# Performance work log

Hardware: AMD Instinct MI355X
Metric: run time of the kernel (lower is better)

The kernel has to match this reference:

```python
import jax, jax.numpy as jnp
import numpy as np

N_NODES = 50000
N_EDGES = 500000
HIDDEN = 128
HEADS = 8
HEAD_DIM = HIDDEN // HEADS


def setup_inputs() -> dict:
    key = jax.random.key(0)
    ks = jax.random.split(key, 20)

    def lin_w(k, fin, fout):
        return (jax.random.normal(k, (fin, fout), jnp.float32) / np.sqrt(fin)).astype(jnp.float32)

    inp = {
        "h": jax.random.normal(ks[0], (N_NODES, HIDDEN), jnp.float32),
        "x": jax.random.normal(ks[1], (N_NODES, 3), jnp.float32),
        "src": jax.random.randint(ks[2], (N_EDGES,), 0, N_NODES, jnp.int32),
        "dst": jax.random.randint(ks[3], (N_EDGES,), 0, N_NODES, jnp.int32),
        "distances": jax.random.uniform(ks[4], (N_EDGES,), jnp.float32),
        # linear layers stored as [in, out] (transposed vs torch nn.Linear)
        "Wq": lin_w(ks[5], HIDDEN, HIDDEN), "bq": jnp.zeros((HIDDEN,), jnp.float32),
        "Wk": lin_w(ks[6], HIDDEN, HIDDEN), "bk": jnp.zeros((HIDDEN,), jnp.float32),
        "Wv": lin_w(ks[7], HIDDEN, HIDDEN), "bv": jnp.zeros((HIDDEN,), jnp.float32),
        "Wo": lin_w(ks[8], HIDDEN, HIDDEN), "bo": jnp.zeros((HIDDEN,), jnp.float32),
        "Wd": lin_w(ks[9], 1, HEADS), "bd": jnp.zeros((HEADS,), jnp.float32),
        "Wg1": lin_w(ks[10], HIDDEN, HIDDEN), "bg1": jnp.zeros((HIDDEN,), jnp.float32),
        "Wg2": lin_w(ks[11], HIDDEN, 1), "bg2": jnp.zeros((1,), jnp.float32),
    }
    return inp


def reference(h, x, src, dst, distances,
              Wq, bq, Wk, bk, Wv, bv, Wo, bo, Wd, bd, Wg1, bg1, Wg2, bg2):
    n = h.shape[0]
    heads = Wd.shape[1]
    dh = Wq.shape[1] // heads

    q = (h @ Wq + bq).reshape(n, heads, dh)
    k = (h @ Wk + bk).reshape(n, heads, dh)
    v = (h @ Wv + bv).reshape(n, heads, dh)

    q_src = q[src]            # [E, heads, dh]
    k_dst = k[dst]
    v_dst = v[dst]

    logits = jnp.einsum('ehd,ehd->eh', q_src, k_dst) / jnp.sqrt(jnp.asarray(dh, h.dtype))
    bias = (distances * distances)[:, None] @ Wd + bd      # [E, heads]
    lg = logits - bias

    # segment softmax over edges grouped by src node
    m = jax.ops.segment_max(lg, src, num_segments=n)        # [N, heads]
    ex = jnp.exp(lg - m[src])
    s = jax.ops.segment_sum(ex, src, num_segments=n)
    w = ex / jnp.maximum(s[src], 1e-9)                      # [E, heads]

    h_upd = jax.ops.segment_sum(v_dst * w[:, :, None], src, num_segments=n)
    h_out = h + h_upd.reshape(n, heads * dh) @ Wo + bo

    w_mean = w.mean(axis=1)                                 # mean over heads -> [E]
    disp = jax.ops.segment_sum((x[dst] - x[src]) * w_mean[:, None], src, num_segments=n)

    gate = jnp.tanh(jax.nn.silu(h_out @ Wg1 + bg1) @ Wg2 + bg2)  # [N, 1]
    x_out = x + gate * disp
    return (h_out, x_out)
```

## Files before the change

kernel.cpp:

```cpp
#include <hip/hip_runtime.h>
#include <math.h>

#define N_NODES 50000
#define N_EDGES 500000
#define HIDDEN 128
#define HEADS 8
#define HEAD_DIM 16

typedef __attribute__((ext_vector_type(8))) short short8;
typedef __attribute__((ext_vector_type(4))) float floatx4;
typedef __attribute__((ext_vector_type(4))) unsigned short ushort4v;

#define OFF_Q       0u
#define OFF_KV      6400000u
#define OFF_HHI     12800000u
#define OFF_HLO     16000000u
#define OFF_DISP    19200000u
#define OFF_CNT     19350016u
#define OFF_ROWPTR  19400032u
#define OFF_CURSOR  19450048u
#define OFF_ESD     19500064u
#define OFF_WSPLIT  20500064u

static __device__ __forceinline__ unsigned short f2bf(float f) {
    unsigned u = __builtin_bit_cast(unsigned, f);
    unsigned r = (u + 0x7FFFu + ((u >> 16) & 1u)) >> 16;
    return (unsigned short)r;
}
static __device__ __forceinline__ float bf2f(unsigned short s) {
    return __builtin_bit_cast(float, (unsigned)s << 16);
}

__global__ void k_zero_int(int* __restrict__ p, int n) {
    int i = blockIdx.x * 256 + threadIdx.x;
    if (i < n) p[i] = 0;
}

__global__ __launch_bounds__(256) void k_split_h(
    const float* __restrict__ h,
    unsigned short* __restrict__ hhi, unsigned short* __restrict__ hlo) {
    int i = (blockIdx.x * 256 + threadIdx.x) * 4;
    float4 xv = *(const float4*)(h + i);
    ushort4v hi, lo;
    float v0[4] = {xv.x, xv.y, xv.z, xv.w};
#pragma unroll
    for (int j = 0; j < 4; ++j) {
        unsigned short a = f2bf(v0[j]);
        hi[j] = a;
        lo[j] = f2bf(v0[j] - bf2f(a));
    }
    *(ushort4v*)(hhi + i) = hi;
    *(ushort4v*)(hlo + i) = lo;
}

__global__ void k_split_w(const float* __restrict__ Wq, const float* __restrict__ Wk,
                          const float* __restrict__ Wv, const float* __restrict__ Wo,
                          const float* __restrict__ Wg1, unsigned short* __restrict__ ws) {
    int t = blockIdx.x * 256 + threadIdx.x;
    int m = t >> 14, r = t & 16383;
    int k = r >> 7, n = r & 127;
    const float* W = (m == 0) ? Wq : (m == 1) ? Wk : (m == 2) ? Wv : (m == 3) ? Wo : Wg1;
    float x = W[k * 128 + n];
    int kc = k >> 5, kin = k & 31, quad = kin >> 3, j = kin & 7;
    int ct = n >> 4, nin = n & 15, lane = quad * 16 + nin;
    unsigned base = ((((unsigned)(m * 4 + kc) * 8 + ct) * 2) * 64 + lane) * 8 + j;
    unsigned short a = f2bf(x);
    ws[base] = a;
    ws[base + 512] = f2bf(x - bf2f(a));
}

__global__ __launch_bounds__(256) void k_qkv_mfma(
    const unsigned short* __restrict__ hhi, const unsigned short* __restrict__ hlo,
    const unsigned short* __restrict__ wsp,
    const float* __restrict__ bq, const float* __restrict__ bk, const float* __restrict__ bv,
    float* __restrict__ q, unsigned* __restrict__ kvp) {
    const int wave = threadIdx.x >> 6, lane = threadIdx.x & 63;
    const int quad = lane >> 4, l15 = lane & 15;
    const int ct0 = wave * 2;
    const int row0 = blockIdx.x * 32;

    floatx4 acc[3][2][2];
#pragma unroll
    for (int m = 0; m < 3; ++m)
#pragma unroll
        for (int c = 0; c < 2; ++c)
#pragma unroll
            for (int r = 0; r < 2; ++r) acc[m][c][r] = (floatx4){0.f, 0.f, 0.f, 0.f};

#pragma unroll
    for (int kc = 0; kc < 4; ++kc) {
        short8 ah[2], al[2];
#pragma unroll
        for (int rt = 0; rt < 2; ++rt) {
            int row = row0 + rt * 16 + l15;
            if (row >= N_NODES) row = N_NODES - 1;
            size_t off = (size_t)row * 128 + kc * 32 + quad * 8;
            ah[rt] = *(const short8*)(hhi + off);
            al[rt] = *(const short8*)(hlo + off);
        }
#pragma unroll
        for (int m = 0; m < 3; ++m) {
#pragma unroll
            for (int ctl = 0; ctl < 2; ++ctl) {
                unsigned fb = ((((unsigned)(m * 4 + kc) * 8 + (ct0 + ctl)) * 2) * 64 + lane) * 8;
                short8 bh = *(const short8*)(wsp + fb);
                short8 bl = *(const short8*)(wsp + fb + 512);
#pragma unroll
                for (int rt = 0; rt < 2; ++rt) {
                    acc[m][ctl][rt] = __builtin_amdgcn_mfma_f32_16x16x32_bf16(
                        ah[rt], bh, acc[m][ctl][rt], 0, 0, 0);
                    acc[m][ctl][rt] = __builtin_amdgcn_mfma_f32_16x16x32_bf16(
                        ah[rt], bl, acc[m][ctl][rt], 0, 0, 0);
                    acc[m][ctl][rt] = __builtin_amdgcn_mfma_f32_16x16x32_bf16(
                        al[rt], bh, acc[m][ctl][rt], 0, 0, 0);
                }
            }
        }
    }

#pragma unroll
    for (int ctl = 0; ctl < 2; ++ctl) {
        int col = (ct0 + ctl) * 16 + l15;
        float bq_ = bq[col], bk_ = bk[col], bv_ = bv[col];
#pragma unroll
        for (int rt = 0; rt < 2; ++rt) {
#pragma unroll
            for (int reg = 0; reg < 4; ++reg) {
                int row = row0 + rt * 16 + quad * 4 + reg;
                if (row < N_NODES) {
                    q[(size_t)row * 128 + col] = acc[0][ctl][rt][reg] + bq_;
                    unsigned kb = f2bf(acc[1][ctl][rt][reg] + bk_);
                    unsigned vb = f2bf(acc[2][ctl][rt][reg] + bv_);
                    kvp[(size_t)row * 128 + col] = kb | (vb << 16);
                }
            }
        }
    }
}

__global__ void k_count(const int* __restrict__ src, int* __restrict__ cnt) {
    int e = blockIdx.x * 256 + threadIdx.x;
    if (e < N_EDGES) atomicAdd(&cnt[src[e]], 1);
}

__global__ __launch_bounds__(1024) void k_scan1(const int* __restrict__ cnt,
                                                int* __restrict__ loc,
                                                int* __restrict__ bsum, int n) {
    __shared__ int buf[1024];
    int t = threadIdx.x;
    int i = blockIdx.x * 1024 + t;
    int val = (i < n) ? cnt[i] : 0;
    buf[t] = val;
    __syncthreads();
    for (int off = 1; off < 1024; off <<= 1) {
        int a = (t >= off) ? buf[t - off] : 0;
        __syncthreads();
        buf[t] += a;
        __syncthreads();
    }
    if (i < n) loc[i] = buf[t];
    if (t == 1023) bsum[blockIdx.x] = buf[1023];
}

__global__ void k_scan2(int* __restrict__ bsum, int nb) {
    int t = threadIdx.x;
    int v = (t < nb) ? bsum[t] : 0;
    for (int off = 1; off < 64; off <<= 1) {
        int a = __shfl_up(v, off);
        if (t >= off) v += a;
    }
    if (t < nb) bsum[t] = v;
}

__global__ void k_scan3(const int* __restrict__ cnt, const int* __restrict__ loc,
                        const int* __restrict__ bsum,
                        int* __restrict__ rowptr, int* __restrict__ cursor, int n) {
    int i = blockIdx.x * 256 + threadIdx.x;
    if (i < n) {
        int off = (i >= 1024) ? bsum[(i >> 10) - 1] : 0;
        int incl = loc[i] + off;
        rowptr[i + 1] = incl;
        cursor[i] = incl - cnt[i];
    }
    if (i == 0) rowptr[0] = 0;
}

__global__ void k_scatter(const int* __restrict__ src, const int* __restrict__ dst,
                          const float* __restrict__ dist, int* __restrict__ cursor,
                          int2* __restrict__ esd) {
    int e = blockIdx.x * 256 + threadIdx.x;
    if (e < N_EDGES) {
        int pos = atomicAdd(&cursor[src[e]], 1);
        float dd = dist[e];
        esd[pos] = make_int2(dst[e], __float_as_int(dd * dd));
    }
}

__global__ __launch_bounds__(256) void k_edge_node(
    const float* __restrict__ q, const unsigned* __restrict__ kvp,
    const float* __restrict__ x,
    const int2* __restrict__ esd, const int* __restrict__ rowptr,
    const float* __restrict__ Wd, const float* __restrict__ bd,
    unsigned short* __restrict__ hupd_hi, unsigned short* __restrict__ hupd_lo,
    float* __restrict__ disp) {
    const int wave = threadIdx.x >> 6, lane = threadIdx.x & 63;
    const int node = blockIdx.x * 4 + wave;
    const int h = lane >> 3, sub = lane & 7;
    const int beg = rowptr[node], end = rowptr[node + 1];

    const float2 qv = *(const float2*)(q + (size_t)node * 128 + 2 * lane);
    const float wdh = Wd[h], bdh = bd[h];
    const bool dal = (sub < 3);
    float xs = dal ? x[node * 3 + sub] : 0.f;
    const unsigned colo = 2 * lane;

    float acc0 = 0.f, acc1 = 0.f, s_own = 0.f, da = 0.f;

    for (int cb = beg; cb < end; cb += 64) {
        int idx = cb + lane;
        int dvec = 0; float d2vec = 0.f;
        if (idx < end) {
            int2 ed = esd[idx];
            dvec = ed.x;
            d2vec = __int_as_float(ed.y);
        }
        int clen = min(64, end - cb);
        int i = 0;
        for (; i + 4 <= clen; i += 4) {
            int di[4]; float dd2[4]; uint2 kv2[4]; float xg[4];
#pragma unroll
            for (int j = 0; j < 4; ++j) {
                di[j]  = __shfl(dvec, i + j);
                dd2[j] = __shfl(d2vec, i + j);
            }
#pragma unroll
            for (int j = 0; j < 4; ++j)
                kv2[j] = *(const uint2*)(kvp + (unsigned)di[j] * 128u + colo);
#pragma unroll
            for (int j = 0; j < 4; ++j)
                xg[j] = dal ? x[(unsigned)di[j] * 3u + sub] : 0.f;
#pragma unroll
            for (int j = 0; j < 4; ++j) {
                float k0 = __builtin_bit_cast(float, kv2[j].x << 16);
                float v0 = __builtin_bit_cast(float, kv2[j].x & 0xFFFF0000u);
                float k1 = __builtin_bit_cast(float, kv2[j].y << 16);
                float v1 = __builtin_bit_cast(float, kv2[j].y & 0xFFFF0000u);
                float p = qv.x * k0 + qv.y * k1;
                p += __shfl_xor(p, 1);
                p += __shfl_xor(p, 2);
                p += __shfl_xor(p, 4);
                float w = __expf(p * 0.25f - (dd2[j] * wdh + bdh));
                s_own += w;
                acc0 += v0 * w;
                acc1 += v1 * w;
                da += (xg[j] - xs) * w;
            }
        }
        for (; i < clen; ++i) {
            int dij  = __shfl(dvec, i);
            float d2 = __shfl(d2vec, i);
            uint2 kv2 = *(const uint2*)(kvp + (unsigned)dij * 128u + colo);
            float xgj = dal ? x[(unsigned)dij * 3u + sub] : 0.f;
            float k0 = __builtin_bit_cast(float, kv2.x << 16);
            float v0 = __builtin_bit_cast(float, kv2.x & 0xFFFF0000u);
            float k1 = __builtin_bit_cast(float, kv2.y << 16);
            float v1 = __builtin_bit_cast(float, kv2.y & 0xFFFF0000u);
            float p = qv.x * k0 + qv.y * k1;
            p += __shfl_xor(p, 1);
            p += __shfl_xor(p, 2);
            p += __shfl_xor(p, 4);
            float w = __expf(p * 0.25f - (d2 * wdh + bdh));
            s_own += w;
            acc0 += v0 * w;
            acc1 += v1 * w;
            da += (xgj - xs) * w;
        }
    }

    float inva = 1.f / fmaxf(s_own, 1e-9f);
    float o0 = acc0 * inva, o1 = acc1 * inva;
    unsigned short h0 = f2bf(o0), h1 = f2bf(o1);
    unsigned short l0 = f2bf(o0 - bf2f(h0)), l1 = f2bf(o1 - bf2f(h1));
    ((unsigned*)hupd_hi)[(size_t)node * 64 + lane] = (unsigned)h0 | ((unsigned)h1 << 16);
    ((unsigned*)hupd_lo)[(size_t)node * 64 + lane] = (unsigned)l0 | ((unsigned)l1 << 16);

    da *= 0.125f * inva;
    da += __shfl_xor(da, 8);
    da += __shfl_xor(da, 16);
    da += __shfl_xor(da, 32);
    if (lane < 3) disp[node * 3 + lane] = da;
}

__global__ __launch_bounds__(256) void k_hout_gate(
    const float* __restrict__ h,
    const unsigned short* __restrict__ hupd_hi, const unsigned short* __restrict__ hupd_lo,
    const unsigned short* __restrict__ wsp,
    const float* __restrict__ bo, const float* __restrict__ bg1,
    const float* __restrict__ Wg2, const float* __restrict__ bg2,
    const float* __restrict__ x, const float* __restrict__ disp,
    float* __restrict__ hout, float* __restrict__ xout) {
    __shared__ float hb[4][16 * 132];
    const int wave = threadIdx.x >> 6, lane = threadIdx.x & 63;
    const int quad = lane >> 4, l15 = lane & 15;
    const int row0 = blockIdx.x * 64 + wave * 16;
    float* hbw = hb[wave];

    floatx4 acc[8];
#pragma unroll
    for (int c = 0; c < 8; ++c) acc[c] = (floatx4){0.f, 0.f, 0.f, 0.f};
#pragma unroll
    for (int kc = 0; kc < 4; ++kc) {
        int row = row0 + l15;
        if (row >= N_NODES) row = N_NODES - 1;
        size_t aoff = (size_t)row * 128 + kc * 32 + quad * 8;
        short8 ah = *(const short8*)(hupd_hi + aoff);
        short8 al = *(const short8*)(hupd_lo + aoff);
#pragma unroll
        for (int ct = 0; ct < 8; ++ct) {
            unsigned fb = ((((unsigned)(3 * 4 + kc) * 8 + ct) * 2) * 64 + lane) * 8;
            short8 bh = *(const short8*)(wsp + fb);
            short8 bl = *(const short8*)(wsp + fb + 512);
            acc[ct] = __builtin_amdgcn_mfma_f32_16x16x32_bf16(ah, bh, acc[ct], 0, 0, 0);
            acc[ct] = __builtin_amdgcn_mfma_f32_16x16x32_bf16(ah, bl, acc[ct], 0, 0, 0);
            acc[ct] = __builtin_amdgcn_mfma_f32_16x16x32_bf16(al, bh, acc[ct], 0, 0, 0);
        }
    }

#pragma unroll
    for (int ct = 0; ct < 8; ++ct) {
        int col = ct * 16 + l15;
        float bias = bo[col];
#pragma unroll
        for (int reg = 0; reg < 4; ++reg) {
            int row = row0 + quad * 4 + reg;
            float val = acc[ct][reg] + bias;
            if (row < N_NODES) {
                val += h[(size_t)row * 128 + col];
                hout[(size_t)row * 128 + col] = val;
            }
            hbw[(quad * 4 + reg) * 132 + col] = val;
        }
    }
    __asm__ volatile("s_waitcnt lgkmcnt(0)" ::: "memory");

    floatx4 acc2[8];
#pragma unroll
    for (int c = 0; c < 8; ++c) acc2[c] = (floatx4){0.f, 0.f, 0.f, 0.f};
#pragma unroll
    for (int kc = 0; kc < 4; ++kc) {
        const float* ap = hbw + l15 * 132 + kc * 32 + quad * 8;
        float4 f0 = *(const float4*)(ap);
        float4 f1 = *(const float4*)(ap + 4);
        float fv[8] = {f0.x, f0.y, f0.z, f0.w, f1.x, f1.y, f1.z, f1.w};
        short8 ah, al;
#pragma unroll
        for (int j = 0; j < 8; ++j) {
            unsigned short hi = f2bf(fv[j]);
            ah[j] = (short)hi;
            al[j] = (short)f2bf(fv[j] - bf2f(hi));
        }
#pragma unroll
        for (int ct = 0; ct < 8; ++ct) {
            unsigned fb = ((((unsigned)(4 * 4 + kc) * 8 + ct) * 2) * 64 + lane) * 8;
            short8 bh = *(const short8*)(wsp + fb);
            short8 bl = *(const short8*)(wsp + fb + 512);
            acc2[ct] = __builtin_amdgcn_mfma_f32_16x16x32_bf16(ah, bh, acc2[ct], 0, 0, 0);
            acc2[ct] = __builtin_amdgcn_mfma_f32_16x16x32_bf16(ah, bl, acc2[ct], 0, 0, 0);
            acc2[ct] = __builtin_amdgcn_mfma_f32_16x16x32_bf16(al, bh, acc2[ct], 0, 0, 0);
        }
    }

    float pr[4] = {0.f, 0.f, 0.f, 0.f};
#pragma unroll
    for (int ct = 0; ct < 8; ++ct) {
        int col = ct * 16 + l15;
        float b1 = bg1[col];
        float w2 = Wg2[col];
#pragma unroll
        for (int reg = 0; reg < 4; ++reg) {
            float z = acc2[ct][reg] + b1;
            pr[reg] += (z / (1.f + __expf(-z))) * w2;
        }
    }
#pragma unroll
    for (int off = 1; off < 16; off <<= 1) {
#pragma unroll
        for (int reg = 0; reg < 4; ++reg) pr[reg] += __shfl_xor(pr[reg], off);
    }
    if (l15 == 0) {
        float b2 = bg2[0];
#pragma unroll
        for (int reg = 0; reg < 4; ++reg) {
            int row = row0 + quad * 4 + reg;
            if (row < N_NODES) {
                float g = tanhf(pr[reg] + b2);
#pragma unroll
                for (int dd = 0; dd < 3; ++dd) {
                    int oo = row * 3 + dd;
                    xout[oo] = x[oo] + g * disp[oo];
                }
            }
        }
    }
}

extern "C" void kernel_launch(void* const* d_in, const int* in_sizes, int n_in,
                              void* d_out, int out_size, void* d_ws, size_t ws_size,
                              hipStream_t stream) {
    const float* h    = (const float*)d_in[0];
    const float* x    = (const float*)d_in[1];
    const int*   src  = (const int*)d_in[2];
    const int*   dst  = (const int*)d_in[3];
    const float* dist = (const float*)d_in[4];
    const float* Wq = (const float*)d_in[5];  const float* bq = (const float*)d_in[6];
    const float* Wk = (const float*)d_in[7];  const float* bk = (const float*)d_in[8];
    const float* Wv = (const float*)d_in[9];  const float* bv = (const float*)d_in[10];
    const float* Wo = (const float*)d_in[11]; const float* bo = (const float*)d_in[12];
    const float* Wd = (const float*)d_in[13]; const float* bd = (const float*)d_in[14];
    const float* Wg1 = (const float*)d_in[15]; const float* bg1 = (const float*)d_in[16];
    const float* Wg2 = (const float*)d_in[17]; const float* bg2 = (const float*)d_in[18];

    float* ws    = (float*)d_ws;
    float* q     = ws + OFF_Q;
    unsigned* kvp = (unsigned*)(ws + OFF_KV);
    float* disp  = ws + OFF_DISP;
    int* cnt     = (int*)(ws + OFF_CNT);
    int* rowptr  = (int*)(ws + OFF_ROWPTR);
    int* cursor  = (int*)(ws + OFF_CURSOR);
    int2* esd    = (int2*)(ws + OFF_ESD);
    unsigned short* hhi = (unsigned short*)(ws + OFF_HHI);
    unsigned short* hlo = (unsigned short*)(ws + OFF_HLO);
    unsigned short* wsp = (unsigned short*)(ws + OFF_WSPLIT);
    int* loc    = (int*)(ws + OFF_Q);
    int* bsum   = (int*)(ws + OFF_Q + 500000u);
    unsigned short* hupd_hi = (unsigned short*)(ws + OFF_HHI);
    unsigned short* hupd_lo = (unsigned short*)(ws + OFF_HLO);
    float* hout = (float*)d_out;
    float* xout = hout + (size_t)N_NODES * HIDDEN;

    const int nscan = (N_NODES + 1023) / 1024;

    k_split_h<<<6250, 256, 0, stream>>>(h, hhi, hlo);
    k_split_w<<<320, 256, 0, stream>>>(Wq, Wk, Wv, Wo, Wg1, wsp);
    k_zero_int<<<(N_NODES + 255) / 256, 256, 0, stream>>>(cnt, N_NODES);
    k_count<<<(N_EDGES + 255) / 256, 256, 0, stream>>>(src, cnt);
    k_scan1<<<nscan, 1024, 0, stream>>>(cnt, loc, bsum, N_NODES);
    k_scan2<<<1, 64, 0, stream>>>(bsum, nscan);
    k_scan3<<<(N_NODES + 255) / 256, 256, 0, stream>>>(cnt, loc, bsum, rowptr, cursor, N_NODES);
    k_scatter<<<(N_EDGES + 255) / 256, 256, 0, stream>>>(src, dst, dist, cursor, esd);
    k_qkv_mfma<<<(N_NODES + 31) / 32, 256, 0, stream>>>(hhi, hlo, wsp, bq, bk, bv, q, kvp);
    k_edge_node<<<N_NODES / 4, 256, 0, stream>>>(q, kvp, x, esd, rowptr,
                                                 Wd, bd, hupd_hi, hupd_lo, disp);
    k_hout_gate<<<(N_NODES + 63) / 64, 256, 0, stream>>>(h, hupd_hi, hupd_lo, wsp,
                                                         bo, bg1, Wg2, bg2,
                                                         x, disp, hout, xout);
}
```

Baseline: 293.3 us.

## Fuse h bf16 split into QKV GEMM and enlarge per-wave row tiles

Drops the separate k_split_h kernel and converts h from fp32 to hi/lo bf16 inside the QKV MFMA kernel. This removes one launch and a full write and read of the split h buffers. The QKV kernel now does 64 rows per block and the output/gate kernel does 32 rows per wave with 128-thread blocks, so each weight fragment load feeds more MFMAs. The edge gather loop is unrolled from 4 to 8 to keep more loads in flight. Together these raise register pressure and may lower occupancy.

```diff
diff --git a/kernel.cpp b/kernel.cpp
--- a/kernel.cpp
+++ b/kernel.cpp
@@ -9,7 +9,6 @@
 
 typedef __attribute__((ext_vector_type(8))) short short8;
 typedef __attribute__((ext_vector_type(4))) float floatx4;
-typedef __attribute__((ext_vector_type(4))) unsigned short ushort4v;
 
 #define OFF_Q       0u
 #define OFF_KV      6400000u
@@ -34,23 +33,6 @@
 __global__ void k_zero_int(int* __restrict__ p, int n) {
     int i = blockIdx.x * 256 + threadIdx.x;
     if (i < n) p[i] = 0;
-}
-
-__global__ __launch_bounds__(256) void k_split_h(
-    const float* __restrict__ h,
-    unsigned short* __restrict__ hhi, unsigned short* __restrict__ hlo) {
-    int i = (blockIdx.x * 256 + threadIdx.x) * 4;
-    float4 xv = *(const float4*)(h + i);
-    ushort4v hi, lo;
-    float v0[4] = {xv.x, xv.y, xv.z, xv.w};
-#pragma unroll
-    for (int j = 0; j < 4; ++j) {
-        unsigned short a = f2bf(v0[j]);
-        hi[j] = a;
-        lo[j] = f2bf(v0[j] - bf2f(a));
-    }
-    *(ushort4v*)(hhi + i) = hi;
-    *(ushort4v*)(hlo + i) = lo;
 }
 
 __global__ void k_split_w(const float* __restrict__ Wq, const float* __restrict__ Wk,
@@ -70,33 +52,39 @@
 }
 
 __global__ __launch_bounds__(256) void k_qkv_mfma(
-    const unsigned short* __restrict__ hhi, const unsigned short* __restrict__ hlo,
-    const unsigned short* __restrict__ wsp,
+    const float* __restrict__ h, const unsigned short* __restrict__ wsp,
     const float* __restrict__ bq, const float* __restrict__ bk, const float* __restrict__ bv,
     float* __restrict__ q, unsigned* __restrict__ kvp) {
     const int wave = threadIdx.x >> 6, lane = threadIdx.x & 63;
     const int quad = lane >> 4, l15 = lane & 15;
     const int ct0 = wave * 2;
-    const int row0 = blockIdx.x * 32;
-
-    floatx4 acc[3][2][2];
+    const int row0 = blockIdx.x * 64;
+
+    floatx4 acc[3][2][4];
 #pragma unroll
     for (int m = 0; m < 3; ++m)
 #pragma unroll
         for (int c = 0; c < 2; ++c)
 #pragma unroll
-            for (int r = 0; r < 2; ++r) acc[m][c][r] = (floatx4){0.f, 0.f, 0.f, 0.f};
+            for (int r = 0; r < 4; ++r) acc[m][c][r] = (floatx4){0.f, 0.f, 0.f, 0.f};
 
 #pragma unroll
     for (int kc = 0; kc < 4; ++kc) {
-        short8 ah[2], al[2];
-#pragma unroll
-        for (int rt = 0; rt < 2; ++rt) {
+        short8 ah[4], al[4];
+#pragma unroll
+        for (int rt = 0; rt < 4; ++rt) {
             int row = row0 + rt * 16 + l15;
             if (row >= N_NODES) row = N_NODES - 1;
-            size_t off = (size_t)row * 128 + kc * 32 + quad * 8;
-            ah[rt] = *(const short8*)(hhi + off);
-            al[rt] = *(const short8*)(hlo + off);
+            const float* hp = h + (size_t)row * 128 + kc * 32 + quad * 8;
+            float4 f0 = *(const float4*)(hp);
+            float4 f1 = *(const float4*)(hp + 4);
+            float fv[8] = {f0.x, f0.y, f0.z, f0.w, f1.x, f1.y, f1.z, f1.w};
+#pragma unroll
+            for (int j = 0; j < 8; ++j) {
+                unsigned short hi = f2bf(fv[j]);
+                ah[rt][j] = (short)hi;
+                al[rt][j] = (short)f2bf(fv[j] - bf2f(hi));
+            }
         }
 #pragma unroll
         for (int m = 0; m < 3; ++m) {
@@ -106,7 +94,7 @@
                 short8 bh = *(const short8*)(wsp + fb);
                 short8 bl = *(const short8*)(wsp + fb + 512);
 #pragma unroll
-                for (int rt = 0; rt < 2; ++rt) {
+                for (int rt = 0; rt < 4; ++rt) {
                     acc[m][ctl][rt] = __builtin_amdgcn_mfma_f32_16x16x32_bf16(
                         ah[rt], bh, acc[m][ctl][rt], 0, 0, 0);
                     acc[m][ctl][rt] = __builtin_amdgcn_mfma_f32_16x16x32_bf16(
@@ -123,7 +111,7 @@
         int col = (ct0 + ctl) * 16 + l15;
         float bq_ = bq[col], bk_ = bk[col], bv_ = bv[col];
 #pragma unroll
-        for (int rt = 0; rt < 2; ++rt) {
+        for (int rt = 0; rt < 4; ++rt) {
 #pragma unroll
             for (int reg = 0; reg < 4; ++reg) {
                 int row = row0 + rt * 16 + quad * 4 + reg;
@@ -226,21 +214,21 @@
         }
         int clen = min(64, end - cb);
         int i = 0;
-        for (; i + 4 <= clen; i += 4) {
-            int di[4]; float dd2[4]; uint2 kv2[4]; float xg[4];
-#pragma unroll
-            for (int j = 0; j < 4; ++j) {
+        for (; i + 8 <= clen; i += 8) {
+            int di[8]; float dd2[8]; uint2 kv2[8]; float xg[8];
+#pragma unroll
+            for (int j = 0; j < 8; ++j) {
                 di[j]  = __shfl(dvec, i + j);
                 dd2[j] = __shfl(d2vec, i + j);
             }
 #pragma unroll
-            for (int j = 0; j < 4; ++j)
+            for (int j = 0; j < 8; ++j)
                 kv2[j] = *(const uint2*)(kvp + (unsigned)di[j] * 128u + colo);
 #pragma unroll
-            for (int j = 0; j < 4; ++j)
+            for (int j = 0; j < 8; ++j)
                 xg[j] = dal ? x[(unsigned)di[j] * 3u + sub] : 0.f;
 #pragma unroll
-            for (int j = 0; j < 4; ++j) {
+            for (int j = 0; j < 8; ++j) {
                 float k0 = __builtin_bit_cast(float, kv2[j].x << 16);
                 float v0 = __builtin_bit_cast(float, kv2[j].x & 0xFFFF0000u);
                 float k1 = __builtin_bit_cast(float, kv2[j].y << 16);
@@ -291,7 +279,7 @@
     if (lane < 3) disp[node * 3 + lane] = da;
 }
 
-__global__ __launch_bounds__(256) void k_hout_gate(
+__global__ __launch_bounds__(128) void k_hout_gate(
     const float* __restrict__ h,
     const unsigned short* __restrict__ hupd_hi, const unsigned short* __restrict__ hupd_lo,
     const unsigned short* __restrict__ wsp,
@@ -299,30 +287,39 @@
     const float* __restrict__ Wg2, const float* __restrict__ bg2,
     const float* __restrict__ x, const float* __restrict__ disp,
     float* __restrict__ hout, float* __restrict__ xout) {
-    __shared__ float hb[4][16 * 132];
+    __shared__ float hb[2][32 * 132];
     const int wave = threadIdx.x >> 6, lane = threadIdx.x & 63;
     const int quad = lane >> 4, l15 = lane & 15;
-    const int row0 = blockIdx.x * 64 + wave * 16;
+    const int rowW = blockIdx.x * 64 + wave * 32;
     float* hbw = hb[wave];
 
-    floatx4 acc[8];
-#pragma unroll
-    for (int c = 0; c < 8; ++c) acc[c] = (floatx4){0.f, 0.f, 0.f, 0.f};
+    floatx4 acc[8][2];
+#pragma unroll
+    for (int c = 0; c < 8; ++c)
+#pragma unroll
+        for (int r = 0; r < 2; ++r) acc[c][r] = (floatx4){0.f, 0.f, 0.f, 0.f};
 #pragma unroll
     for (int kc = 0; kc < 4; ++kc) {
-        int row = row0 + l15;
-        if (row >= N_NODES) row = N_NODES - 1;
-        size_t aoff = (size_t)row * 128 + kc * 32 + quad * 8;
-        short8 ah = *(const short8*)(hupd_hi + aoff);
-        short8 al = *(const short8*)(hupd_lo + aoff);
+        short8 ah[2], al[2];
+#pragma unroll
+        for (int rt = 0; rt < 2; ++rt) {
+            int row = rowW + rt * 16 + l15;
+            if (row >= N_NODES) row = N_NODES - 1;
+            size_t aoff = (size_t)row * 128 + kc * 32 + quad * 8;
+            ah[rt] = *(const short8*)(hupd_hi + aoff);
+            al[rt] = *(const short8*)(hupd_lo + aoff);
+        }
 #pragma unroll
         for (int ct = 0; ct < 8; ++ct) {
             unsigned fb = ((((unsigned)(3 * 4 + kc) * 8 + ct) * 2) * 64 + lane) * 8;
             short8 bh = *(const short8*)(wsp + fb);
             short8 bl = *(const short8*)(wsp + fb + 512);
-            acc[ct] = __builtin_amdgcn_mfma_f32_16x16x32_bf16(ah, bh, acc[ct], 0, 0, 0);
-            acc[ct] = __builtin_amdgcn_mfma_f32_16x16x32_bf16(ah, bl, acc[ct], 0, 0, 0);
-            acc[ct] = __builtin_amdgcn_mfma_f32_16x16x32_bf16(al, bh, acc[ct], 0, 0, 0);
+#pragma unroll
+            for (int rt = 0; rt < 2; ++rt) {
+                acc[ct][rt] = __builtin_amdgcn_mfma_f32_16x16x32_bf16(ah[rt], bh, acc[ct][rt], 0, 0, 0);
+                acc[ct][rt] = __builtin_amdgcn_mfma_f32_16x16x32_bf16(ah[rt], bl, acc[ct][rt], 0, 0, 0);
+                acc[ct][rt] = __builtin_amdgcn_mfma_f32_16x16x32_bf16(al[rt], bh, acc[ct][rt], 0, 0, 0);
+            }
         }
     }
 
@@ -331,73 +328,92 @@
         int col = ct * 16 + l15;
         float bias = bo[col];
 #pragma unroll
-        for (int reg = 0; reg < 4; ++reg) {
-            int row = row0 + quad * 4 + reg;
-            float val = acc[ct][reg] + bias;
-            if (row < N_NODES) {
-                val += h[(size_t)row * 128 + col];
-                hout[(size_t)row * 128 + col] = val;
-            }
-            hbw[(quad * 4 + reg) * 132 + col] = val;
+        for (int rt = 0; rt < 2; ++rt) {
+#pragma unroll
+            for (int reg = 0; reg < 4; ++reg) {
+                int row = rowW + rt * 16 + quad * 4 + reg;
+                float val = acc[ct][rt][reg] + bias;
+                if (row < N_NODES) {
+                    val += h[(size_t)row * 128 + col];
+                    hout[(size_t)row * 128 + col] = val;
+                }
+                hbw[(rt * 16 + quad * 4 + reg) * 132 + col] = val;
+            }
         }
     }
     __asm__ volatile("s_waitcnt lgkmcnt(0)" ::: "memory");
 
-    floatx4 acc2[8];
-#pragma unroll
-    for (int c = 0; c < 8; ++c) acc2[c] = (floatx4){0.f, 0.f, 0.f, 0.f};
+    floatx4 acc2[8][2];
+#pragma unroll
+    for (int c = 0; c < 8; ++c)
+#pragma unroll
+        for (int r = 0; r < 2; ++r) acc2[c][r] = (floatx4){0.f, 0.f, 0.f, 0.f};
 #pragma unroll
     for (int kc = 0; kc < 4; ++kc) {
-        const float* ap = hbw + l15 * 132 + kc * 32 + quad * 8;
-        float4 f0 = *(const float4*)(ap);
-        float4 f1 = *(const float4*)(ap + 4);
-        float fv[8] = {f0.x, f0.y, f0.z, f0.w, f1.x, f1.y, f1.z, f1.w};
-        short8 ah, al;
-#pragma unroll
-        for (int j = 0; j < 8; ++j) {
-            unsigned short hi = f2bf(fv[j]);
-            ah[j] = (short)hi;
-            al[j] = (short)f2bf(fv[j] - bf2f(hi));
+        short8 ah2[2], al2[2];
+#pragma unroll
+        for (int rt = 0; rt < 2; ++rt) {
+            const float* ap = hbw + (rt * 16 + l15) * 132 + kc * 32 + quad * 8;
+            float4 f0 = *(const float4*)(ap);
+            float4 f1 = *(const float4*)(ap + 4);
+            float fv[8] = {f0.x, f0.y, f0.z, f0.w, f1.x, f1.y, f1.z, f1.w};
+#pragma unroll
+            for (int j = 0; j < 8; ++j) {
+                unsigned short hi = f2bf(fv[j]);
+                ah2[rt][j] = (short)hi;
+                al2[rt][j] = (short)f2bf(fv[j] - bf2f(hi));
+            }
         }
 #pragma unroll
         for (int ct = 0; ct < 8; ++ct) {
             unsigned fb = ((((unsigned)(4 * 4 + kc) * 8 + ct) * 2) * 64 + lane) * 8;
             short8 bh = *(const short8*)(wsp + fb);
             short8 bl = *(const short8*)(wsp + fb + 512);
-            acc2[ct] = __builtin_amdgcn_mfma_f32_16x16x32_bf16(ah, bh, acc2[ct], 0, 0, 0);
-            acc2[ct] = __builtin_amdgcn_mfma_f32_16x16x32_bf16(ah, bl, acc2[ct], 0, 0, 0);
-            acc2[ct] = __builtin_amdgcn_mfma_f32_16x16x32_bf16(al, bh, acc2[ct], 0, 0, 0);
-        }
-    }
-
-    float pr[4] = {0.f, 0.f, 0.f, 0.f};
+#pragma unroll
+            for (int rt = 0; rt < 2; ++rt) {
+                acc2[ct][rt] = __builtin_amdgcn_mfma_f32_16x16x32_bf16(ah2[rt], bh, acc2[ct][rt], 0, 0, 0);
+                acc2[ct][rt] = __builtin_amdgcn_mfma_f32_16x16x32_bf16(ah2[rt], bl, acc2[ct][rt], 0, 0, 0);
+                acc2[ct][rt] = __builtin_amdgcn_mfma_f32_16x16x32_bf16(al2[rt], bh, acc2[ct][rt], 0, 0, 0);
+            }
+        }
+    }
+
+    float pr[2][4] = {{0.f, 0.f, 0.f, 0.f}, {0.f, 0.f, 0.f, 0.f}};
 #pragma unroll
     for (int ct = 0; ct < 8; ++ct) {
         int col = ct * 16 + l15;
         float b1 = bg1[col];
         float w2 = Wg2[col];
 #pragma unroll
-        for (int reg = 0; reg < 4; ++reg) {
-            float z = acc2[ct][reg] + b1;
-            pr[reg] += (z / (1.f + __expf(-z))) * w2;
+        for (int rt = 0; rt < 2; ++rt) {
+#pragma unroll
+            for (int reg = 0; reg < 4; ++reg) {
+                float z = acc2[ct][rt][reg] + b1;
+                pr[rt][reg] += (z / (1.f + __expf(-z))) * w2;
+            }
         }
     }
 #pragma unroll
     for (int off = 1; off < 16; off <<= 1) {
 #pragma unroll
-        for (int reg = 0; reg < 4; ++reg) pr[reg] += __shfl_xor(pr[reg], off);
+        for (int rt = 0; rt < 2; ++rt)
+#pragma unroll
+            for (int reg = 0; reg < 4; ++reg) pr[rt][reg] += __shfl_xor(pr[rt][reg], off);
     }
     if (l15 == 0) {
         float b2 = bg2[0];
 #pragma unroll
-        for (int reg = 0; reg < 4; ++reg) {
-            int row = row0 + quad * 4 + reg;
-            if (row < N_NODES) {
-                float g = tanhf(pr[reg] + b2);
-#pragma unroll
-                for (int dd = 0; dd < 3; ++dd) {
-                    int oo = row * 3 + dd;
-                    xout[oo] = x[oo] + g * disp[oo];
+        for (int rt = 0; rt < 2; ++rt) {
+#pragma unroll
+            for (int reg = 0; reg < 4; ++reg) {
+                int row = rowW + rt * 16 + quad * 4 + reg;
+                if (row < N_NODES) {
+                    float g = tanhf(pr[rt][reg] + b2);
+#pragma unroll
+                    for (int dd = 0; dd < 3; ++dd) {
+                        int oo = row * 3 + dd;
+                        xout[oo] = x[oo] + g * disp[oo];
+                    }
                 }
             }
         }
@@ -428,8 +444,6 @@
     int* rowptr  = (int*)(ws + OFF_ROWPTR);
     int* cursor  = (int*)(ws + OFF_CURSOR);
     int2* esd    = (int2*)(ws + OFF_ESD);
-    unsigned short* hhi = (unsigned short*)(ws + OFF_HHI);
-    unsigned short* hlo = (unsigned short*)(ws + OFF_HLO);
     unsigned short* wsp = (unsigned short*)(ws + OFF_WSPLIT);
     int* loc    = (int*)(ws + OFF_Q);
     int* bsum   = (int*)(ws + OFF_Q + 500000u);
@@ -440,7 +454,6 @@
 
     const int nscan = (N_NODES + 1023) / 1024;
 
-    k_split_h<<<6250, 256, 0, stream>>>(h, hhi, hlo);
     k_split_w<<<320, 256, 0, stream>>>(Wq, Wk, Wv, Wo, Wg1, wsp);
     k_zero_int<<<(N_NODES + 255) / 256, 256, 0, stream>>>(cnt, N_NODES);
     k_count<<<(N_EDGES + 255) / 256, 256, 0, stream>>>(src, cnt);
@@ -448,10 +461,10 @@
     k_scan2<<<1, 64, 0, stream>>>(bsum, nscan);
     k_scan3<<<(N_NODES + 255) / 256, 256, 0, stream>>>(cnt, loc, bsum, rowptr, cursor, N_NODES);
     k_scatter<<<(N_EDGES + 255) / 256, 256, 0, stream>>>(src, dst, dist, cursor, esd);
-    k_qkv_mfma<<<(N_NODES + 31) / 32, 256, 0, stream>>>(hhi, hlo, wsp, bq, bk, bv, q, kvp);
+    k_qkv_mfma<<<(N_NODES + 63) / 64, 256, 0, stream>>>(h, wsp, bq, bk, bv, q, kvp);
     k_edge_node<<<N_NODES / 4, 256, 0, stream>>>(q, kvp, x, esd, rowptr,
                                                  Wd, bd, hupd_hi, hupd_lo, disp);
-    k_hout_gate<<<(N_NODES + 63) / 64, 256, 0, stream>>>(h, hupd_hi, hupd_lo, wsp,
+    k_hout_gate<<<(N_NODES + 63) / 64, 128, 0, stream>>>(h, hupd_hi, hupd_lo, wsp,
                                                          bo, bg1, Wg2, bg2,
                                                          x, disp, hout, xout);
 }
```

Measured after the change: 302.3 us. 3.1% more time.
